# Kernel tuning notes

Measured on AMD Instinct MI355X. Metric: run time of the kernel, lower is better.

Reference implementation:

```python
import jax, jax.numpy as jnp
import numpy as np

N_NODES = 100000
N_EDGES = 3200000
IN_DIM = 128
HID_DIM = 64
OUT_DIM = 2
N_GRAPHS = 512


def setup_inputs() -> dict:
    key = jax.random.key(0)
    ks = jax.random.split(key, 8)
    x = jax.random.normal(ks[0], (N_NODES, IN_DIM), dtype=jnp.float32)
    edge_index = jax.random.randint(ks[1], (2, N_EDGES), 0, N_NODES, dtype=jnp.int64)
    batch = jnp.sort(jax.random.randint(ks[2], (N_NODES,), 0, N_GRAPHS, dtype=jnp.int64))
    # GCNConv params (glorot-ish scale)
    W_gcn = jax.random.normal(ks[3], (IN_DIM, HID_DIM), dtype=jnp.float32) / np.sqrt(IN_DIM)
    b_gcn = jnp.zeros((HID_DIM,), dtype=jnp.float32)
    # MLP params: Linear(hid,hid) -> ReLU -> Linear(hid,out)
    W1 = jax.random.normal(ks[4], (HID_DIM, HID_DIM), dtype=jnp.float32) / np.sqrt(HID_DIM)
    b1 = jnp.zeros((HID_DIM,), dtype=jnp.float32)
    W2 = jax.random.normal(ks[5], (HID_DIM, OUT_DIM), dtype=jnp.float32) / np.sqrt(HID_DIM)
    b2 = jnp.zeros((OUT_DIM,), dtype=jnp.float32)
    return {"x": x, "edge_index": edge_index, "batch": batch,
            "W_gcn": W_gcn, "b_gcn": b_gcn, "W1": W1, "b1": b1, "W2": W2, "b2": b2}


def reference(x, edge_index, batch, W_gcn, b_gcn, W1, b1, W2, b2):
    n = x.shape[0]
    # --- GCNConv: add self-loops, symmetric normalization, aggregate, transform ---
    self_loop = jnp.arange(n, dtype=edge_index.dtype)
    row = jnp.concatenate([edge_index[0], self_loop])  # source nodes
    col = jnp.concatenate([edge_index[1], self_loop])  # target nodes
    deg = jax.ops.segment_sum(jnp.ones_like(col, dtype=x.dtype), col, num_segments=n)
    dinv = jnp.where(deg > 0, jax.lax.rsqrt(deg), 0.0)
    norm = dinv[row] * dinv[col]                       # (E+N,)
    xw = x @ W_gcn                                     # (N, hid) transform first (in_dim > hid)
    msg = xw[row] * norm[:, None]                      # gather + scale
    z = jax.ops.segment_sum(msg, col, num_segments=n) + b_gcn  # scatter-add
    z = jax.nn.relu(z)
    # --- global mean pool over graphs ---
    sums = jax.ops.segment_sum(z, batch, num_segments=N_GRAPHS)          # (G, hid)
    cnts = jax.ops.segment_sum(jnp.ones((n,), z.dtype), batch, num_segments=N_GRAPHS)
    g = sums / jnp.maximum(cnts, 1.0)[:, None]
    # --- MLP -> sigmoid ---
    h = jax.nn.relu(g @ W1 + b1)
    return jax.nn.sigmoid(h @ W2 + b2)                 # (G, out_dim)
```

## Files before the change

### kernel.cpp

```cpp
#include <hip/hip_runtime.h>

#define N_NODES 100000
#define N_EDGES 3200000
#define IN_DIM 128
#define HID_DIM 64
#define OUT_DIM 2
#define N_GRAPHS 512

#define BSHIFT 6
#define NBK 1563
#define NBB 1024
#define EPB2 3125
#define CAPSHIFT 12
#define LDS_E2 2816
#define ZERO_ROW N_NODES

__device__ inline unsigned short f2bf(float f) {
    union { float f; unsigned int i; } v; v.f = f;
    unsigned int r = v.i + 0x7fffu + ((v.i >> 16) & 1u);
    return (unsigned short)(r >> 16);
}

typedef __attribute__((ext_vector_type(8))) short bf16x8;
typedef __attribute__((ext_vector_type(4))) float f32x4;
typedef __attribute__((ext_vector_type(2))) float f32x2;

__global__ __launch_bounds__(1024) void k_init(float* __restrict__ gsum,
                                               int* __restrict__ cnt_g,
                                               float* __restrict__ gcnt,
                                               unsigned char* __restrict__ xws) {
    int b = blockIdx.x, t = threadIdx.x;
    if (b < 32) {
        gsum[b * 1024 + t] = 0.f;
    } else if (b < 34) {
        int j = (b - 32) * 1024 + t;
        if (j < NBK) cnt_g[j] = 0;
    } else {
        if (t < N_GRAPHS) gcnt[t] = 0.f;
        if (t >= 1008)
            ((int*)(xws + (size_t)ZERO_ROW * HID_DIM))[t - 1008] = 0;
    }
}

__global__ __launch_bounds__(512) void k_bin(const int* __restrict__ row,
                                             const int* __restrict__ col,
                                             int* __restrict__ cnt_g,
                                             int* __restrict__ binned) {
    __shared__ int h[NBK];
    __shared__ int cur[NBK];
    for (int i = threadIdx.x; i < NBK; i += 512) { h[i] = 0; cur[i] = 0; }
    __syncthreads();
    int s = blockIdx.x * EPB2, e = s + EPB2;
    for (int i = s + threadIdx.x; i < e; i += 512)
        atomicAdd(&h[col[i] >> BSHIFT], 1);
    __syncthreads();
    for (int i = threadIdx.x; i < NBK; i += 512) {
        int hv = h[i];
        if (hv) h[i] = (i << CAPSHIFT) + atomicAdd(&cnt_g[i], hv);
    }
    __syncthreads();
    for (int i = s + threadIdx.x; i < e; i += 512) {
        int c = col[i];
        int r = row[i];
        int bk = c >> BSHIFT;
        int rk = atomicAdd(&cur[bk], 1);
        binned[h[bk] + rk] = ((c & 63) << 17) | r;
    }
}

__global__ __launch_bounds__(256) void k_gemm(const float* __restrict__ x,
                                              const float* __restrict__ Wg,
                                              const int* __restrict__ cnt_g,
                                              const int* __restrict__ binned,
                                              int* __restrict__ degs,
                                              unsigned char* __restrict__ xws) {
    __shared__ unsigned short wb[16][64][8];
    __shared__ int cnt[64];

    if (threadIdx.x < 64) cnt[threadIdx.x] = 0;
    for (int idx = threadIdx.x; idx < 1024; idx += 256) {
        int f = idx >> 6, l = idx & 63;
        int ks = f >> 2, nt = f & 3;
        int n = (l & 15) + (nt << 4);
        int kbase = (ks << 5) + ((l >> 4) << 3);
        unsigned short tmp[8];
#pragma unroll
        for (int j = 0; j < 8; j++)
            tmp[j] = f2bf(Wg[(kbase + j) * HID_DIM + n]);
        *(bf16x8*)&wb[f][l][0] = *(const bf16x8*)tmp;
    }
    __syncthreads();

    int bkt = blockIdx.x;
    int m = cnt_g[bkt];
    for (int i = threadIdx.x; i < m; i += 256)
        atomicAdd(&cnt[binned[(bkt << CAPSHIFT) + i] >> 17], 1);

    int wave = threadIdx.x >> 6;
    int lane = threadIdx.x & 63;
    int q = lane >> 4, nn = lane & 15;

    bf16x8 bfrag[4][4];
#pragma unroll
    for (int ks = 0; ks < 4; ks++)
#pragma unroll
        for (int nt = 0; nt < 4; nt++)
            bfrag[ks][nt] = *(const bf16x8*)&wb[ks * 4 + nt][lane][0];

    int node0 = bkt * 64 + wave * 16;
    int arow = node0 + nn;
    if (arow > N_NODES - 1) arow = N_NODES - 1;
    const float* xrow = x + (size_t)arow * IN_DIM + (q << 3);

    f32x4 acc[4] = {{0.f,0.f,0.f,0.f},{0.f,0.f,0.f,0.f},
                    {0.f,0.f,0.f,0.f},{0.f,0.f,0.f,0.f}};
#pragma unroll
    for (int ks = 0; ks < 4; ks++) {
        float4 xa = *(const float4*)(xrow + ks * 32);
        float4 xb_ = *(const float4*)(xrow + ks * 32 + 4);
        bf16x8 af;
        af[0] = (short)f2bf(xa.x); af[1] = (short)f2bf(xa.y);
        af[2] = (short)f2bf(xa.z); af[3] = (short)f2bf(xa.w);
        af[4] = (short)f2bf(xb_.x); af[5] = (short)f2bf(xb_.y);
        af[6] = (short)f2bf(xb_.z); af[7] = (short)f2bf(xb_.w);
#pragma unroll
        for (int nt = 0; nt < 4; nt++)
            acc[nt] = __builtin_amdgcn_mfma_f32_16x16x32_bf16(af, bfrag[ks][nt], acc[nt], 0, 0, 0);
    }
    __syncthreads();

    if (threadIdx.x < 64) degs[bkt * 64 + threadIdx.x] = cnt[threadIdx.x];

#pragma unroll
    for (int r = 0; r < 4; r++) {
        int lrow = wave * 16 + q * 4 + r;
        int mrow = bkt * 64 + lrow;
        if (mrow < N_NODES) {
            float dn = rsqrtf((float)cnt[lrow] + 1.0f);
            int p01 = __builtin_amdgcn_cvt_pk_fp8_f32(acc[0][r] * dn, acc[1][r] * dn, 0, false);
            int p23 = __builtin_amdgcn_cvt_pk_fp8_f32(acc[2][r] * dn, acc[3][r] * dn, 0, false);
            unsigned char* rp = xws + (size_t)mrow * HID_DIM + nn;
            rp[0]  = (unsigned char)(p01 & 0xff);
            rp[16] = (unsigned char)((p01 >> 8) & 0xff);
            rp[32] = (unsigned char)(p23 & 0xff);
            rp[48] = (unsigned char)((p23 >> 8) & 0xff);
        }
    }
}

__global__ __launch_bounds__(512) void k_aggrf(const unsigned char* __restrict__ xws,
                                               const int* __restrict__ binned,
                                               const int* __restrict__ cnt_g,
                                               const int* __restrict__ degs,
                                               const int* __restrict__ batch,
                                               const float* __restrict__ bg,
                                               float* __restrict__ gsum,
                                               float* __restrict__ gcnt) {
    int bkt = blockIdx.x;
    int nbase = bkt << BSHIFT;
    int nnodes = N_NODES - nbase; if (nnodes > 64) nnodes = 64;
    int m = cnt_g[bkt];
    int base = bkt << CAPSHIFT;

    __shared__ int cnt[64];
    __shared__ int lptr[65];
    __shared__ int cur[64];
    __shared__ int sb[64];
    __shared__ float gcl[8];
    __shared__ alignas(16) int srt[LDS_E2];
    __shared__ float pool[8][4][64];

    if (threadIdx.x < 64) {
        int n = nbase + threadIdx.x;
        cnt[threadIdx.x] = (threadIdx.x < nnodes) ? degs[bkt * 64 + threadIdx.x] : 0;
        sb[threadIdx.x]  = (threadIdx.x < nnodes) ? batch[n] : 0;
        cur[threadIdx.x] = 0;
    }
    if (threadIdx.x < 8) gcl[threadIdx.x] = 0.f;
    for (int t = threadIdx.x; t < 8 * 4 * 64; t += 512)
        ((float*)pool)[t] = 0.f;
    __syncthreads();

    if (threadIdx.x < 64) {
        int v = (threadIdx.x < nnodes) ? ((cnt[threadIdx.x] + 8) & ~7) : 0;
        int run = v;
#pragma unroll
        for (int off = 1; off < 64; off <<= 1) {
            int t = __shfl_up(run, off);
            if (threadIdx.x >= off) run += t;
        }
        lptr[threadIdx.x + 1] = run;
        if (threadIdx.x == 0) lptr[0] = 0;
    }
    __syncthreads();
    int tot = lptr[64]; if (tot > LDS_E2) tot = LDS_E2;
    for (int i = threadIdx.x; i < tot; i += 512) srt[i] = ZERO_ROW << 6;
    __syncthreads();
    if (threadIdx.x < nnodes) {
        int p = lptr[threadIdx.x] + cnt[threadIdx.x];
        if (p < LDS_E2) srt[p] = (nbase + threadIdx.x) << 6;
        int sl = sb[threadIdx.x] - sb[0];
        if (sl < 8) atomicAdd(&gcl[sl], 1.0f);
        else atomicAdd(&gcnt[sb[threadIdx.x]], 1.0f);
    }
    for (int i = threadIdx.x; i < m; i += 512) {
        int pk = binned[base + i];
        int nid = pk >> 17;
        int rk = atomicAdd(&cur[nid], 1);
        int pos = lptr[nid] + rk;
        if (pos < LDS_E2) srt[pos] = (pk & 0x1FFFF) << 6;
    }
    __syncthreads();

    int wave = threadIdx.x >> 6;
    int lane = threadIdx.x & 63;
    int sub = lane >> 4;
    int lc  = lane & 15;
    int l4  = lc << 2;
    const unsigned char* xbl = xws + l4;
    int g0 = sb[0];
    float4 bia = ((const float4*)bg)[lc];

#pragma unroll
    for (int r = 0; r < 2; r++) {
        int ln = wave * 8 + sub * 2 + r;
        int valid = (ln < nnodes);
        int s0 = valid ? lptr[ln] : 0;
        int e0 = valid ? lptr[ln + 1] : 0;
        if (s0 > LDS_E2) s0 = LDS_E2;
        if (e0 > LDS_E2) e0 = LDS_E2;
        f32x2 al0 = {0.f,0.f}, ah0 = {0.f,0.f};
        f32x2 al1 = {0.f,0.f}, ah1 = {0.f,0.f};
        for (int i = s0; i < e0; i += 8) {
            int4 ra = *(const int4*)&srt[i];
            int4 rb = *(const int4*)&srt[i + 4];
            unsigned int d0 = *(const unsigned int*)(xbl + ra.x);
            unsigned int d1 = *(const unsigned int*)(xbl + ra.y);
            unsigned int d2 = *(const unsigned int*)(xbl + ra.z);
            unsigned int d3 = *(const unsigned int*)(xbl + ra.w);
            unsigned int d4 = *(const unsigned int*)(xbl + rb.x);
            unsigned int d5 = *(const unsigned int*)(xbl + rb.y);
            unsigned int d6 = *(const unsigned int*)(xbl + rb.z);
            unsigned int d7 = *(const unsigned int*)(xbl + rb.w);
            f32x2 p;
            p = __builtin_amdgcn_cvt_pk_f32_fp8(d0, false); al0 += p;
            p = __builtin_amdgcn_cvt_pk_f32_fp8(d0, true);  ah0 += p;
            p = __builtin_amdgcn_cvt_pk_f32_fp8(d1, false); al1 += p;
            p = __builtin_amdgcn_cvt_pk_f32_fp8(d1, true);  ah1 += p;
            p = __builtin_amdgcn_cvt_pk_f32_fp8(d2, false); al0 += p;
            p = __builtin_amdgcn_cvt_pk_f32_fp8(d2, true);  ah0 += p;
            p = __builtin_amdgcn_cvt_pk_f32_fp8(d3, false); al1 += p;
            p = __builtin_amdgcn_cvt_pk_f32_fp8(d3, true);  ah1 += p;
            p = __builtin_amdgcn_cvt_pk_f32_fp8(d4, false); al0 += p;
            p = __builtin_amdgcn_cvt_pk_f32_fp8(d4, true);  ah0 += p;
            p = __builtin_amdgcn_cvt_pk_f32_fp8(d5, false); al1 += p;
            p = __builtin_amdgcn_cvt_pk_f32_fp8(d5, true);  ah1 += p;
            p = __builtin_amdgcn_cvt_pk_f32_fp8(d6, false); al0 += p;
            p = __builtin_amdgcn_cvt_pk_f32_fp8(d6, true);  ah0 += p;
            p = __builtin_amdgcn_cvt_pk_f32_fp8(d7, false); al1 += p;
            p = __builtin_amdgcn_cvt_pk_f32_fp8(d7, true);  ah1 += p;
        }
        f32x2 alo = al0 + al1, ahi = ah0 + ah1;
        int slot = 99;
        float4 val;
        if (valid) {
            float dn = rsqrtf((float)cnt[ln] + 1.0f);
            val.x = fmaxf(alo[0] * dn + bia.x, 0.f);
            val.y = fmaxf(alo[1] * dn + bia.y, 0.f);
            val.z = fmaxf(ahi[0] * dn + bia.z, 0.f);
            val.w = fmaxf(ahi[1] * dn + bia.w, 0.f);
            slot = sb[ln] - g0;
        }
#pragma unroll
        for (int ss = 0; ss < 4; ss++) {
            if (sub == ss && slot < 4) {
                float4* pp = (float4*)&pool[wave][slot][l4];
                float4 pv = *pp;
                pv.x += val.x; pv.y += val.y; pv.z += val.z; pv.w += val.w;
                *pp = pv;
            }
        }
        if (slot >= 4 && slot < 99) {
            float* gp = &gsum[sb[ln] * HID_DIM + l4];
            atomicAdd(gp + 0, val.x); atomicAdd(gp + 1, val.y);
            atomicAdd(gp + 2, val.z); atomicAdd(gp + 3, val.w);
        }
    }
    __syncthreads();

    if (threadIdx.x < 8) {
        float c = gcl[threadIdx.x];
        if (c != 0.f) atomicAdd(&gcnt[g0 + threadIdx.x], c);
    }
    for (int t = threadIdx.x; t < 4 * 64; t += 512) {
        int slot = t >> 6, j = t & 63;
        float v = 0.f;
#pragma unroll
        for (int w2 = 0; w2 < 8; w2++) v += pool[w2][slot][j];
        if (v != 0.f) atomicAdd(&gsum[(g0 + slot) * HID_DIM + j], v);
    }
}

__global__ __launch_bounds__(64) void k_mlp(const float* __restrict__ gsum,
                                            const float* __restrict__ gcnt,
                                            const float* __restrict__ W1,
                                            const float* __restrict__ b1,
                                            const float* __restrict__ W2,
                                            const float* __restrict__ b2,
                                            float* __restrict__ out) {
    int g = blockIdx.x;
    int j = threadIdx.x;
    float cnt = fmaxf(gcnt[g], 1.0f);

    __shared__ float gs[64];
    __shared__ float hs[64];
    gs[j] = gsum[g * 64 + j] / cnt;
    __syncthreads();

    float h = b1[j];
    for (int k = 0; k < 64; k++) h += gs[k] * W1[k * 64 + j];
    hs[j] = fmaxf(h, 0.f);
    __syncthreads();

    if (j < OUT_DIM) {
        float o = b2[j];
        for (int k = 0; k < 64; k++) o += hs[k] * W2[k * OUT_DIM + j];
        out[g * OUT_DIM + j] = 1.f / (1.f + expf(-o));
    }
}

extern "C" void kernel_launch(void* const* d_in, const int* in_sizes, int n_in,
                              void* d_out, int out_size, void* d_ws, size_t ws_size,
                              hipStream_t stream) {
    const float* x   = (const float*)d_in[0];
    const int* eidx  = (const int*)d_in[1];
    const int* batch = (const int*)d_in[2];
    const float* Wg  = (const float*)d_in[3];
    const float* bg  = (const float*)d_in[4];
    const float* W1  = (const float*)d_in[5];
    const float* b1  = (const float*)d_in[6];
    const float* W2  = (const float*)d_in[7];
    const float* b2  = (const float*)d_in[8];
    float* out = (float*)d_out;

    char* w = (char*)d_ws;
    unsigned char* xws = (unsigned char*)w;     w += (size_t)(N_NODES + 1) * HID_DIM;
    int*   binned  = (int*)w;                   w += ((size_t)NBK << CAPSHIFT) * 4;
    int*   cnt_g   = (int*)w;                   w += NBK * 4;
    int*   degs    = (int*)w;                   w += (size_t)NBK * 64 * 4;
    float* gsum    = (float*)w;                 w += N_GRAPHS * HID_DIM * 4;
    float* gcnt    = (float*)w;                 w += N_GRAPHS * 4;

    const int* rowp = eidx;
    const int* colp = eidx + N_EDGES;

    k_init<<<35, 1024, 0, stream>>>(gsum, cnt_g, gcnt, xws);
    k_bin<<<NBB, 512, 0, stream>>>(rowp, colp, cnt_g, binned);
    k_gemm<<<NBK, 256, 0, stream>>>(x, Wg, cnt_g, binned, degs, xws);
    k_aggrf<<<NBK, 512, 0, stream>>>(xws, binned, cnt_g, degs, batch, bg, gsum, gcnt);
    k_mlp<<<N_GRAPHS, 64, 0, stream>>>(gsum, gcnt, W1, b1, W2, b2, out);
}
```

Baseline: 228.9 us.

## Locally sort edges by bucket in LDS before scattering to global bins

The binning kernel now handles twice as many edges per block, with half as many blocks. It computes a block-local prefix scan over the bucket histogram and stages edges in shared memory sorted by bucket. It then writes them to global memory, so each bucket's entries from a block land in consecutive addresses instead of fully random single-element stores. The cost is an extra scan with many barriers, about 58KB more LDS per block (which may reduce occupancy), and an extra pass through shared memory.

```diff
diff --git a/kernel.cpp b/kernel.cpp
--- a/kernel.cpp
+++ b/kernel.cpp
@@ -9,8 +9,8 @@
 
 #define BSHIFT 6
 #define NBK 1563
-#define NBB 1024
-#define EPB2 3125
+#define NBB 512
+#define EPB3 6250
 #define CAPSHIFT 12
 #define LDS_E2 2816
 #define ZERO_ROW N_NODES
@@ -47,24 +47,62 @@
                                              int* __restrict__ cnt_g,
                                              int* __restrict__ binned) {
     __shared__ int h[NBK];
+    __shared__ int lofs[NBK];
     __shared__ int cur[NBK];
-    for (int i = threadIdx.x; i < NBK; i += 512) { h[i] = 0; cur[i] = 0; }
-    __syncthreads();
-    int s = blockIdx.x * EPB2, e = s + EPB2;
-    for (int i = s + threadIdx.x; i < e; i += 512)
+    __shared__ int ps[512];
+    __shared__ int sorted[EPB3];
+    __shared__ unsigned short bkt16[EPB3];
+    int t = threadIdx.x;
+    for (int i = t; i < NBK; i += 512) { h[i] = 0; cur[i] = 0; }
+    __syncthreads();
+    int s = blockIdx.x * EPB3, e = s + EPB3;
+    for (int i = s + t; i < e; i += 512)
         atomicAdd(&h[col[i] >> BSHIFT], 1);
     __syncthreads();
-    for (int i = threadIdx.x; i < NBK; i += 512) {
+    {
+        int b0 = t << 2;
+        int loc[4];
+        int run = 0;
+#pragma unroll
+        for (int j = 0; j < 4; j++) {
+            int b = b0 + j;
+            loc[j] = run;
+            run += (b < NBK) ? h[b] : 0;
+        }
+        ps[t] = run;
+        __syncthreads();
+        for (int off = 1; off < 512; off <<= 1) {
+            int v = (t >= off) ? ps[t - off] : 0;
+            __syncthreads();
+            ps[t] += v;
+            __syncthreads();
+        }
+        int base = (t > 0) ? ps[t - 1] : 0;
+#pragma unroll
+        for (int j = 0; j < 4; j++) {
+            int b = b0 + j;
+            if (b < NBK) lofs[b] = base + loc[j];
+        }
+    }
+    __syncthreads();
+    for (int i = t; i < NBK; i += 512) {
         int hv = h[i];
         if (hv) h[i] = (i << CAPSHIFT) + atomicAdd(&cnt_g[i], hv);
     }
     __syncthreads();
-    for (int i = s + threadIdx.x; i < e; i += 512) {
+    for (int i = s + t; i < e; i += 512) {
         int c = col[i];
         int r = row[i];
         int bk = c >> BSHIFT;
         int rk = atomicAdd(&cur[bk], 1);
-        binned[h[bk] + rk] = ((c & 63) << 17) | r;
+        int p = lofs[bk] + rk;
+        sorted[p] = ((c & 63) << 17) | r;
+        bkt16[p] = (unsigned short)bk;
+    }
+    __syncthreads();
+    for (int i = t; i < EPB3; i += 512) {
+        int bk = bkt16[i];
+        binned[h[bk] + (i - lofs[bk])] = sorted[i];
     }
 }
 
```

New measurement: 192.0 us (median of 2 runs). 16.1% less time.

## Replace single-pass edge binning with two-pass radix binning through super-buckets

Applied to the files above, without the earlier changes.

The single-pass bin kernel, which scattered edges straight into 1563 fine buckets, is split into two passes. The first pass scatters edges into 98 super-buckets using locally sorted indices so that writes are contiguous. The second pass splits each super-bucket into 16 fine buckets. This targets the cost of badly coalesced scattered global writes and heavy atomic contention on many buckets. In exchange it adds an extra read and write of the full edge list plus a kernel launch, and it silently truncates if a super-bucket or quarter overflows its fixed capacity.

```diff
diff --git a/kernel.cpp b/kernel.cpp
--- a/kernel.cpp
+++ b/kernel.cpp
@@ -9,8 +9,10 @@
 
 #define BSHIFT 6
 #define NBK 1563
-#define NBB 1024
-#define EPB2 3125
+#define NSUP 98
+#define SUPCAP 36864
+#define NBS 512
+#define EPS 6250
 #define CAPSHIFT 12
 #define LDS_E2 2816
 #define ZERO_ROW N_NODES
@@ -27,14 +29,17 @@
 
 __global__ __launch_bounds__(1024) void k_init(float* __restrict__ gsum,
                                                int* __restrict__ cnt_g,
+                                               int* __restrict__ scnt,
                                                float* __restrict__ gcnt,
                                                unsigned char* __restrict__ xws) {
     int b = blockIdx.x, t = threadIdx.x;
     if (b < 32) {
         gsum[b * 1024 + t] = 0.f;
-    } else if (b < 34) {
-        int j = (b - 32) * 1024 + t;
-        if (j < NBK) cnt_g[j] = 0;
+    } else if (b == 32) {
+        cnt_g[t] = 0;
+    } else if (b == 33) {
+        if (t < NBK - 1024) cnt_g[1024 + t] = 0;
+        if (t >= 600 && t < 600 + NSUP) scnt[t - 600] = 0;
     } else {
         if (t < N_GRAPHS) gcnt[t] = 0.f;
         if (t >= 1008)
@@ -42,29 +47,89 @@
     }
 }
 
-__global__ __launch_bounds__(512) void k_bin(const int* __restrict__ row,
-                                             const int* __restrict__ col,
-                                             int* __restrict__ cnt_g,
-                                             int* __restrict__ binned) {
-    __shared__ int h[NBK];
-    __shared__ int cur[NBK];
-    for (int i = threadIdx.x; i < NBK; i += 512) { h[i] = 0; cur[i] = 0; }
-    __syncthreads();
-    int s = blockIdx.x * EPB2, e = s + EPB2;
-    for (int i = s + threadIdx.x; i < e; i += 512)
-        atomicAdd(&h[col[i] >> BSHIFT], 1);
-    __syncthreads();
-    for (int i = threadIdx.x; i < NBK; i += 512) {
-        int hv = h[i];
-        if (hv) h[i] = (i << CAPSHIFT) + atomicAdd(&cnt_g[i], hv);
-    }
-    __syncthreads();
-    for (int i = s + threadIdx.x; i < e; i += 512) {
-        int c = col[i];
-        int r = row[i];
-        int bk = c >> BSHIFT;
-        int rk = atomicAdd(&cur[bk], 1);
-        binned[h[bk] + rk] = ((c & 63) << 17) | r;
+__global__ __launch_bounds__(512) void k_super(const int* __restrict__ row,
+                                               const int* __restrict__ col,
+                                               int* __restrict__ scnt,
+                                               int* __restrict__ sup) {
+    __shared__ int h[NSUP];
+    __shared__ int cur[NSUP];
+    __shared__ int lofs[NSUP + 1];
+    __shared__ unsigned short idx16[EPS];
+    int t = threadIdx.x;
+    if (t < NSUP) { h[t] = 0; cur[t] = 0; }
+    __syncthreads();
+    int s = blockIdx.x * EPS;
+    for (int i = t; i < EPS; i += 512)
+        atomicAdd(&h[col[s + i] >> 10], 1);
+    __syncthreads();
+    if (t == 0) {
+        int run = 0;
+        for (int i = 0; i < NSUP; i++) { lofs[i] = run; run += h[i]; }
+        lofs[NSUP] = run;
+    }
+    __syncthreads();
+    if (t < NSUP) {
+        int hv = h[t];
+        if (hv) h[t] = t * SUPCAP + atomicAdd(&scnt[t], hv);
+    }
+    __syncthreads();
+    for (int i = t; i < EPS; i += 512) {
+        int sb = col[s + i] >> 10;
+        int rk = atomicAdd(&cur[sb], 1);
+        idx16[lofs[sb] + rk] = (unsigned short)i;
+    }
+    __syncthreads();
+    for (int i = t; i < EPS; i += 512) {
+        int idx = idx16[i];
+        int c = col[s + idx];
+        int r = row[s + idx];
+        int sb = c >> 10;
+        sup[h[sb] + (i - lofs[sb])] = ((c & 1023) << 17) | r;
+    }
+}
+
+__global__ __launch_bounds__(512) void k_fine(const int* __restrict__ sup,
+                                              const int* __restrict__ scnt,
+                                              int* __restrict__ cnt_g,
+                                              int* __restrict__ binned) {
+    __shared__ int h[16];
+    __shared__ int cur[16];
+    __shared__ int lofs[17];
+    __shared__ int resv[16];
+    __shared__ unsigned short idx16[9216];
+    int sb = blockIdx.x >> 2, q = blockIdx.x & 3;
+    int m = scnt[sb]; if (m > SUPCAP) m = SUPCAP;
+    int qs = (q * m) >> 2, qe = ((q + 1) * m) >> 2;
+    int n = qe - qs; if (n > 9216) n = 9216;
+    int base = sb * SUPCAP + qs;
+    int t = threadIdx.x;
+    if (t < 16) { h[t] = 0; cur[t] = 0; }
+    __syncthreads();
+    for (int i = t; i < n; i += 512)
+        atomicAdd(&h[(sup[base + i] >> 23) & 15], 1);
+    __syncthreads();
+    if (t == 0) {
+        int run = 0;
+        for (int i = 0; i < 16; i++) { lofs[i] = run; run += h[i]; }
+        lofs[16] = run;
+    }
+    __syncthreads();
+    if (t < 16) {
+        int hv = h[t];
+        int fb = (sb << 4) + t;
+        resv[t] = (hv && fb < NBK) ? (fb << CAPSHIFT) + atomicAdd(&cnt_g[fb], hv) : 0;
+    }
+    __syncthreads();
+    for (int i = t; i < n; i += 512) {
+        int fbl = (sup[base + i] >> 23) & 15;
+        int rk = atomicAdd(&cur[fbl], 1);
+        idx16[lofs[fbl] + rk] = (unsigned short)i;
+    }
+    __syncthreads();
+    for (int i = t; i < n; i += 512) {
+        int pk1 = sup[base + idx16[i]];
+        int fbl = (pk1 >> 23) & 15;
+        binned[resv[fbl] + (i - lofs[fbl])] = pk1 & 0x7FFFFF;
     }
 }
 
@@ -345,7 +410,9 @@
 
     char* w = (char*)d_ws;
     unsigned char* xws = (unsigned char*)w;     w += (size_t)(N_NODES + 1) * HID_DIM;
+    int*   sup     = (int*)w;                   w += (size_t)(NSUP + 1) * SUPCAP * 4;
     int*   binned  = (int*)w;                   w += ((size_t)NBK << CAPSHIFT) * 4;
+    int*   scnt    = (int*)w;                   w += NSUP * 4;
     int*   cnt_g   = (int*)w;                   w += NBK * 4;
     int*   degs    = (int*)w;                   w += (size_t)NBK * 64 * 4;
     float* gsum    = (float*)w;                 w += N_GRAPHS * HID_DIM * 4;
@@ -354,8 +421,9 @@
     const int* rowp = eidx;
     const int* colp = eidx + N_EDGES;
 
-    k_init<<<35, 1024, 0, stream>>>(gsum, cnt_g, gcnt, xws);
-    k_bin<<<NBB, 512, 0, stream>>>(rowp, colp, cnt_g, binned);
+    k_init<<<35, 1024, 0, stream>>>(gsum, cnt_g, scnt, gcnt, xws);
+    k_super<<<NBS, 512, 0, stream>>>(rowp, colp, scnt, sup);
+    k_fine<<<NSUP * 4, 512, 0, stream>>>(sup, scnt, cnt_g, binned);
     k_gemm<<<NBK, 256, 0, stream>>>(x, Wg, cnt_g, binned, degs, xws);
     k_aggrf<<<NBK, 512, 0, stream>>>(xws, binned, cnt_g, degs, batch, bg, gsum, gcnt);
     k_mlp<<<N_GRAPHS, 64, 0, stream>>>(gsum, gcnt, W1, b1, W2, b2, out);
```

Result: faster. 210.5 us (-8.0%).
